# Kernel tuning notes

Hardware: AMD Instinct MI355X
Metric: run time of the kernel (lower is better)

## Reference

```python
import jax, jax.numpy as jnp
import numpy as np

B, C, N, DI, DC = 64, 32, 1152, 8, 16
ROUTINGS = 3


def squash(x, axis=-1):
    sq = jnp.sum(x * x, axis=axis, keepdims=True)
    scale = sq / (1.0 + sq) / jnp.sqrt(sq + 1e-07)
    return scale * x


def setup_inputs() -> dict:
    key = jax.random.key(0)
    k1, k2 = jax.random.split(key)
    inputs = jax.random.normal(k1, (B, N, DI), dtype=jnp.float32)
    # Xavier-uniform init for W[n_caps, n_in, d_cap, d_in]; fan computed over last two dims
    limit = float(np.sqrt(6.0 / (DC + DI)))
    W = jax.random.uniform(k2, (C, N, DC, DI), dtype=jnp.float32, minval=-limit, maxval=limit)
    return {"inputs": inputs, "W": W}


def reference(inputs, W):
    # inputs_hat[b,c,n,i] = sum_j W[c,n,i,j] * inputs[b,n,j]
    inputs_hat = jnp.einsum('cnij,bnj->bcni', W, inputs)  # [B,C,N,DC]
    b = jnp.zeros((B, C, N), dtype=inputs_hat.dtype)
    outputs = None
    for i in range(ROUTINGS):
        c = jax.nn.softmax(b, axis=1)                      # over output capsules
        s = jnp.einsum('bcn,bcni->bci', c, inputs_hat)     # weighted sum over input caps
        outputs = squash(s)                                # [B,C,DC]
        if i < ROUTINGS - 1:
            agreement = jnp.einsum('bci,bcni->bcn', outputs, inputs_hat)
            b = b + agreement
    return outputs
```

## Files before the change

kernel.cpp:

```cpp
#include <hip/hip_runtime.h>
#include <hip/hip_bf16.h>

#define B_  64
#define C_  32
#define N_  1152
#define DI_ 8
#define DC_ 16
#define NCH 3
#define NSLOT 128
#define STH 512

static __device__ __forceinline__ unsigned pkbf(float a, float b) {
    __hip_bfloat162 t = __float22bfloat162_rn(make_float2(a, b));
    return *reinterpret_cast<unsigned*>(&t);
}
static __device__ __forceinline__ float ubf_lo(unsigned u) {
    union { unsigned u; float f; } x; x.u = u << 16; return x.f;
}
static __device__ __forceinline__ float ubf_hi(unsigned u) {
    union { unsigned u; float f; } x; x.u = u & 0xffff0000u; return x.f;
}

__global__ __launch_bounds__(STH, 2) void caps_hat(
    const float* __restrict__ X, const float* __restrict__ W,
    uint4* __restrict__ hatg, float* __restrict__ partials)
{
    __shared__ float wlds[NCH * 64 * 64];
    __shared__ float xlds[NCH * 16 * 8];

    const int bg   = blockIdx.x & 3;
    const int slot = blockIdx.x >> 2;
    const int tid  = threadIdx.x;
    const int w    = tid >> 6;
    const int lane = tid & 63;
    const int c    = lane & 31;
    const int h    = lane >> 5;
    const int bl0  = w * 2;
    const int le   = 2 * c + h;
    const int sw   = c & 7;

    float acc[2][8];
#pragma unroll
    for (int bq = 0; bq < 2; bq++)
#pragma unroll
        for (int r = 0; r < 8; r++) acc[bq][r] = 0.f;

    for (int cc = 0; cc < 3; cc++) {
        if (cc) __syncthreads();
        const int n0 = (slot + cc * NSLOT) * NCH;

        for (int G = tid; G < NCH * 1024; G += STH) {
            const int nl = G >> 10, f = (G >> 4) & 63, q = G & 15;
            const int wc = f >> 1, wh = f & 1;
            const float4 v = *(const float4*)(W + (size_t)(wc * N_ + n0 + nl) * 128 + wh * 64 + q * 4);
            *(float4*)(wlds + (nl * 64 + f) * 64 + (q ^ (wc & 7)) * 4) = v;
        }
        if (tid < NCH * 32) {
            const int nl = tid >> 5, bl = (tid >> 1) & 15, qx = tid & 1;
            const float4 v = *(const float4*)(X + (size_t)((bg * 16 + bl) * N_ + n0 + nl) * DI_ + qx * 4);
            *(float4*)(xlds + (nl * 16 + bl) * 8 + qx * 4) = v;
        }
        __syncthreads();

#pragma unroll
        for (int nl = 0; nl < NCH; nl++) {
            float4 xa[2], xb[2];
#pragma unroll
            for (int bq = 0; bq < 2; bq++) {
                const float* xp = xlds + (nl * 16 + bl0 + bq) * 8;
                xa[bq] = *(const float4*)xp;
                xb[bq] = *(const float4*)(xp + 4);
            }
            float hv[2][8];
            const float* frag = wlds + (nl * 64 + le) * 64;
#pragma unroll
            for (int r = 0; r < 8; r++) {
                const int pa = ((2 * r) ^ sw) * 4;
                const int pb = pa ^ 4;
                const float4 wa = *(const float4*)(frag + pa);
                const float4 wb = *(const float4*)(frag + pb);
#pragma unroll
                for (int bq = 0; bq < 2; bq++) {
                    hv[bq][r] = wa.x * xa[bq].x + wa.y * xa[bq].y + wa.z * xa[bq].z + wa.w * xa[bq].w
                              + wb.x * xb[bq].x + wb.y * xb[bq].y + wb.z * xb[bq].z + wb.w * xb[bq].w;
                }
            }
#pragma unroll
            for (int bq = 0; bq < 2; bq++) {
                uint4 hq;
                hq.x = pkbf(hv[bq][0], hv[bq][1]);
                hq.y = pkbf(hv[bq][2], hv[bq][3]);
                hq.z = pkbf(hv[bq][4], hv[bq][5]);
                hq.w = pkbf(hv[bq][6], hv[bq][7]);
                const int b = bg * 16 + bl0 + bq;
                hatg[(size_t)(b * N_ + n0 + nl) * 64 + le] = hq;
#pragma unroll
                for (int r = 0; r < 8; r++) acc[bq][r] += hv[bq][r];
            }
        }
    }

    float* pout = partials + (size_t)(bg * NSLOT + slot) * (16 * 512);
#pragma unroll
    for (int bq = 0; bq < 2; bq++) {
        float* pb = pout + (bl0 + bq) * 512 + le * 8;
        *(float4*)pb       = make_float4(acc[bq][0]*0.03125f, acc[bq][1]*0.03125f,
                                         acc[bq][2]*0.03125f, acc[bq][3]*0.03125f);
        *(float4*)(pb + 4) = make_float4(acc[bq][4]*0.03125f, acc[bq][5]*0.03125f,
                                         acc[bq][6]*0.03125f, acc[bq][7]*0.03125f);
    }
}

__global__ __launch_bounds__(STH, 2) void caps_route(
    const uint4* __restrict__ hatg, const float* __restrict__ accb,
    float* __restrict__ p2)
{
    const int b    = blockIdx.x >> 3;
    const int oct  = blockIdx.x & 7;
    const int tid  = threadIdx.x;
    const int w    = tid >> 6;
    const int lane = tid & 63;
    const int c    = lane & 31;
    const int h    = lane >> 5;
    const int le   = 2 * c + h;

    const float* ap = accb + (size_t)b * 512 + le * 8;
    const float4 a0 = *(const float4*)ap;
    const float4 a1 = *(const float4*)(ap + 4);

    float acc[8] = {0.f,0.f,0.f,0.f,0.f,0.f,0.f,0.f};
    const uint4* hb = hatg + (size_t)(b * N_ + oct * 144) * 64 + le;

    for (int k = 0; k < 6; k++) {
        uint4 v[3];
#pragma unroll
        for (int u = 0; u < 3; u++)
            v[u] = hb[(size_t)(w + 8 * (3 * k + u)) * 64];
#pragma unroll
        for (int u = 0; u < 3; u++) {
            float hv[8];
            hv[0] = ubf_lo(v[u].x); hv[1] = ubf_hi(v[u].x);
            hv[2] = ubf_lo(v[u].y); hv[3] = ubf_hi(v[u].y);
            hv[4] = ubf_lo(v[u].z); hv[5] = ubf_hi(v[u].z);
            hv[6] = ubf_lo(v[u].w); hv[7] = ubf_hi(v[u].w);
            float lg = hv[0]*a0.x + hv[1]*a0.y + hv[2]*a0.z + hv[3]*a0.w
                     + hv[4]*a1.x + hv[5]*a1.y + hv[6]*a1.z + hv[7]*a1.w;
            lg += __shfl_xor(lg, 32, 64);
            const float e = __expf(lg);
            float s = e;
#pragma unroll
            for (int m = 16; m >= 1; m >>= 1) s += __shfl_xor(s, m, 64);
            const float sc = e * __builtin_amdgcn_rcpf(s);
#pragma unroll
            for (int r = 0; r < 8; r++) acc[r] += sc * hv[r];
        }
    }
    float* pb = p2 + ((size_t)(b * 8 + oct) * 8 + w) * 512 + le * 8;
    *(float4*)pb       = make_float4(acc[0], acc[1], acc[2], acc[3]);
    *(float4*)(pb + 4) = make_float4(acc[4], acc[5], acc[6], acc[7]);
}

__global__ __launch_bounds__(256) void caps_r1(
    const float* __restrict__ partials, float* __restrict__ accb,
    float* __restrict__ out, int t)
{
    const int b   = blockIdx.x >> 2;
    const int q   = blockIdx.x & 3;
    const int tid = threadIdx.x;
    const int e   = q * 128 + (tid >> 1);
    const int p   = tid & 1;
    const int bg  = b >> 4, bl = b & 15;
    const float* base = partials + (size_t)bg * NSLOT * 8192 + (size_t)bl * 512 + e;
    float v = 0.f;
#pragma unroll 8
    for (int ch = p; ch < NSLOT; ch += 2)
        v += base[(size_t)ch * 8192];
    v += __shfl_xor(v, 1, 64);
    float sq = v * v;
#pragma unroll
    for (int m = 2; m <= 16; m <<= 1) sq += __shfl_xor(sq, m, 64);
    const float scale = sq / (1.f + sq) * rsqrtf(sq + 1e-7f);
    const float ov = v * scale;
    if (p == 0) {
        const int oidx = b * 512 + e;
        if (t == 2) out[oidx] = ov;
        else        accb[oidx] = (t == 0) ? ov : (accb[oidx] + ov);
    }
}

__global__ __launch_bounds__(512) void caps_r2(
    const float* __restrict__ p2, float* __restrict__ accb,
    float* __restrict__ out, int t)
{
    const int b = blockIdx.x;
    const int e = threadIdx.x;
    const float* base = p2 + (size_t)b * 32768 + e;
    float v = 0.f;
#pragma unroll 16
    for (int s = 0; s < 64; s++) v += base[s * 512];
    float sq = v * v;
#pragma unroll
    for (int m = 1; m <= 8; m <<= 1) sq += __shfl_xor(sq, m, 64);
    const float scale = sq / (1.f + sq) * rsqrtf(sq + 1e-7f);
    const float ov = v * scale;
    const int oidx = b * 512 + e;
    if (t == 2) out[oidx] = ov;
    else        accb[oidx] += ov;
}

__global__ __launch_bounds__(STH, 2) void caps_s_fb(
    const float* __restrict__ X, const float* __restrict__ W,
    const float* __restrict__ aout, float* __restrict__ partials, int t)
{
    __shared__ float wlds[NCH * 64 * 64];
    __shared__ float xlds[NCH * 16 * 8];
    const int bg = blockIdx.x & 3, slot = blockIdx.x >> 2;
    const int tid = threadIdx.x, w = tid >> 6, lane = tid & 63;
    const int c = lane & 31, h = lane >> 5, bl0 = w * 2, sw = c & 7;
    float areg[2][8] = {};
    if (t > 0) {
#pragma unroll
        for (int bq = 0; bq < 2; bq++) {
            const float* ap = aout + (size_t)(bg * 16 + bl0 + bq) * 512 + c * 16 + h * 8;
            const float4 a0 = *(const float4*)ap; const float4 a1 = *(const float4*)(ap + 4);
            areg[bq][0]=a0.x; areg[bq][1]=a0.y; areg[bq][2]=a0.z; areg[bq][3]=a0.w;
            areg[bq][4]=a1.x; areg[bq][5]=a1.y; areg[bq][6]=a1.z; areg[bq][7]=a1.w;
        }
    }
    float acc[2][8];
#pragma unroll
    for (int bq = 0; bq < 2; bq++)
#pragma unroll
        for (int r = 0; r < 8; r++) acc[bq][r] = 0.f;
    for (int cc = 0; cc < 3; cc++) {
        if (cc) __syncthreads();
        const int n0 = (slot + cc * NSLOT) * NCH;
        for (int G = tid; G < NCH * 1024; G += STH) {
            const int nl = G >> 10, f = (G >> 4) & 63, q = G & 15;
            const int wc = f >> 1, wh = f & 1;
            const float4 v = *(const float4*)(W + (size_t)(wc * N_ + n0 + nl) * 128 + wh * 64 + q * 4);
            *(float4*)(wlds + (nl * 64 + f) * 64 + (q ^ (wc & 7)) * 4) = v;
        }
        if (tid < NCH * 32) {
            const int nl = tid >> 5, bl = (tid >> 1) & 15, qx = tid & 1;
            const float4 v = *(const float4*)(X + (size_t)((bg * 16 + bl) * N_ + n0 + nl) * DI_ + qx * 4);
            *(float4*)(xlds + (nl * 16 + bl) * 8 + qx * 4) = v;
        }
        __syncthreads();
#pragma unroll
        for (int nl = 0; nl < NCH; nl++) {
            float4 xa[2], xb[2];
#pragma unroll
            for (int bq = 0; bq < 2; bq++) {
                const float* xp = xlds + (nl * 16 + bl0 + bq) * 8;
                xa[bq] = *(const float4*)xp; xb[bq] = *(const float4*)(xp + 4);
            }
            float hat[2][8];
            const float* frag = wlds + (nl * 64 + 2 * c + h) * 64;
#pragma unroll
            for (int r = 0; r < 8; r++) {
                const int pa = ((2 * r) ^ sw) * 4; const int pb = pa ^ 4;
                const float4 wa = *(const float4*)(frag + pa);
                const float4 wb = *(const float4*)(frag + pb);
#pragma unroll
                for (int bq = 0; bq < 2; bq++)
                    hat[bq][r] = wa.x*xa[bq].x + wa.y*xa[bq].y + wa.z*xa[bq].z + wa.w*xa[bq].w
                               + wb.x*xb[bq].x + wb.y*xb[bq].y + wb.z*xb[bq].z + wb.w*xb[bq].w;
            }
#pragma unroll
            for (int bq = 0; bq < 2; bq++) {
                float softc;
                if (t > 0) {
                    float lg = hat[bq][0]*areg[bq][0] + hat[bq][1]*areg[bq][1]
                             + hat[bq][2]*areg[bq][2] + hat[bq][3]*areg[bq][3]
                             + hat[bq][4]*areg[bq][4] + hat[bq][5]*areg[bq][5]
                             + hat[bq][6]*areg[bq][6] + hat[bq][7]*areg[bq][7];
                    lg += __shfl_xor(lg, 32, 64);
                    const float e = __expf(lg);
                    float s = e;
#pragma unroll
                    for (int m = 16; m >= 1; m >>= 1) s += __shfl_xor(s, m, 64);
                    softc = e / s;
                } else softc = 1.0f / 32.0f;
#pragma unroll
                for (int r = 0; r < 8; r++) acc[bq][r] += softc * hat[bq][r];
            }
        }
    }
    float* pout = partials + (size_t)(bg * NSLOT + slot) * (16 * 512);
#pragma unroll
    for (int bq = 0; bq < 2; bq++) {
        float* pb = pout + (bl0 + bq) * 512 + c * 16 + h * 8;
        *(float4*)pb       = make_float4(acc[bq][0], acc[bq][1], acc[bq][2], acc[bq][3]);
        *(float4*)(pb + 4) = make_float4(acc[bq][4], acc[bq][5], acc[bq][6], acc[bq][7]);
    }
}

extern "C" void kernel_launch(void* const* d_in, const int* in_sizes, int n_in,
                              void* d_out, int out_size, void* d_ws, size_t ws_size,
                              hipStream_t stream) {
    const float* X = (const float*)d_in[0];
    const float* W = (const float*)d_in[1];
    float* out = (float*)d_out;

    const size_t hat_b = (size_t)B_ * N_ * 512 * 2;
    const size_t p1_b  = (size_t)512 * 8192 * 4;
    const size_t p2_b  = (size_t)B_ * 64 * 512 * 4;
    const size_t acc_b = (size_t)B_ * 512 * 4;

    if (ws_size >= hat_b + p1_b + p2_b + acc_b) {
        char* ws = (char*)d_ws;
        uint4* hatg = (uint4*)ws;
        float* p1   = (float*)(ws + hat_b);
        float* p2   = (float*)(ws + hat_b + p1_b);
        float* accb = (float*)(ws + hat_b + p1_b + p2_b);
        caps_hat  <<<512, STH, 0, stream>>>(X, W, hatg, p1);
        caps_r1   <<<256, 256, 0, stream>>>(p1, accb, out, 0);
        caps_route<<<512, STH, 0, stream>>>(hatg, accb, p2);
        caps_r2   <<<64, 512, 0, stream>>>(p2, accb, out, 1);
        caps_route<<<512, STH, 0, stream>>>(hatg, accb, p2);
        caps_r2   <<<64, 512, 0, stream>>>(p2, accb, out, 2);
    } else {
        float* partials = (float*)d_ws;
        float* accb = partials + (size_t)512 * 8192;
        for (int t = 0; t < 3; t++) {
            caps_s_fb<<<512, STH, 0, stream>>>(X, W, accb, partials, t);
            caps_r1  <<<256, 256, 0, stream>>>(partials, accb, out, t);
        }
    }
}
```

Baseline: 153.4 us.

## Store hat in fp16, double batch per block, reduce route partials in LDS

The cached inputs_hat is now stored as fp16 instead of bf16, and caps_hat processes 32 batches per block (4 per wave) over half as many blocks. This halves the W tile loads from global memory and raises per-load reuse. caps_route reduces its 8 wave partials in shared memory before writing, and its occupancy hint rises to 6. That shrinks p2 writes and the r2 reduction eightfold. The costs are more registers in caps_hat, fewer blocks to fill the GPU, and fp16 range and precision limits on hat values.

```diff
diff --git a/kernel.cpp b/kernel.cpp
--- a/kernel.cpp
+++ b/kernel.cpp
@@ -1,5 +1,6 @@
 #include <hip/hip_runtime.h>
 #include <hip/hip_bf16.h>
+#include <hip/hip_fp16.h>
 
 #define B_  64
 #define C_  32
@@ -10,38 +11,36 @@
 #define NSLOT 128
 #define STH 512
 
-static __device__ __forceinline__ unsigned pkbf(float a, float b) {
-    __hip_bfloat162 t = __float22bfloat162_rn(make_float2(a, b));
+static __device__ __forceinline__ unsigned pkh(float a, float b) {
+    __half2 t = __float22half2_rn(make_float2(a, b));
     return *reinterpret_cast<unsigned*>(&t);
 }
-static __device__ __forceinline__ float ubf_lo(unsigned u) {
-    union { unsigned u; float f; } x; x.u = u << 16; return x.f;
-}
-static __device__ __forceinline__ float ubf_hi(unsigned u) {
-    union { unsigned u; float f; } x; x.u = u & 0xffff0000u; return x.f;
+static __device__ __forceinline__ float2 uph(unsigned u) {
+    __half2 h; *reinterpret_cast<unsigned*>(&h) = u;
+    return __half22float2(h);
 }
 
 __global__ __launch_bounds__(STH, 2) void caps_hat(
     const float* __restrict__ X, const float* __restrict__ W,
-    uint4* __restrict__ hatg, float* __restrict__ partials)
+    uint4* __restrict__ hatg, float* __restrict__ p1)
 {
     __shared__ float wlds[NCH * 64 * 64];
-    __shared__ float xlds[NCH * 16 * 8];
-
-    const int bg   = blockIdx.x & 3;
-    const int slot = blockIdx.x >> 2;
+    __shared__ float xlds[NCH * 32 * 8];
+
+    const int bg   = blockIdx.x & 1;
+    const int slot = blockIdx.x >> 1;
     const int tid  = threadIdx.x;
     const int w    = tid >> 6;
     const int lane = tid & 63;
     const int c    = lane & 31;
     const int h    = lane >> 5;
-    const int bl0  = w * 2;
+    const int bl0  = w * 4;
     const int le   = 2 * c + h;
     const int sw   = c & 7;
 
-    float acc[2][8];
-#pragma unroll
-    for (int bq = 0; bq < 2; bq++)
+    float acc[4][8];
+#pragma unroll
+    for (int bq = 0; bq < 4; bq++)
 #pragma unroll
         for (int r = 0; r < 8; r++) acc[bq][r] = 0.f;
 
@@ -55,54 +54,57 @@
             const float4 v = *(const float4*)(W + (size_t)(wc * N_ + n0 + nl) * 128 + wh * 64 + q * 4);
             *(float4*)(wlds + (nl * 64 + f) * 64 + (q ^ (wc & 7)) * 4) = v;
         }
-        if (tid < NCH * 32) {
-            const int nl = tid >> 5, bl = (tid >> 1) & 15, qx = tid & 1;
-            const float4 v = *(const float4*)(X + (size_t)((bg * 16 + bl) * N_ + n0 + nl) * DI_ + qx * 4);
-            *(float4*)(xlds + (nl * 16 + bl) * 8 + qx * 4) = v;
+        if (tid < NCH * 64) {
+            const int nl = tid >> 6, bl = (tid >> 1) & 31, qx = tid & 1;
+            const float4 v = *(const float4*)(X + (size_t)((bg * 32 + bl) * N_ + n0 + nl) * DI_ + qx * 4);
+            *(float4*)(xlds + (nl * 32 + bl) * 8 + qx * 4) = v;
         }
         __syncthreads();
 
 #pragma unroll
         for (int nl = 0; nl < NCH; nl++) {
-            float4 xa[2], xb[2];
-#pragma unroll
-            for (int bq = 0; bq < 2; bq++) {
-                const float* xp = xlds + (nl * 16 + bl0 + bq) * 8;
+            float4 xa[4], xb[4];
+#pragma unroll
+            for (int bq = 0; bq < 4; bq++) {
+                const float* xp = xlds + (nl * 32 + bl0 + bq) * 8;
                 xa[bq] = *(const float4*)xp;
                 xb[bq] = *(const float4*)(xp + 4);
             }
-            float hv[2][8];
+            uint4 hq[4];
             const float* frag = wlds + (nl * 64 + le) * 64;
 #pragma unroll
-            for (int r = 0; r < 8; r++) {
-                const int pa = ((2 * r) ^ sw) * 4;
-                const int pb = pa ^ 4;
-                const float4 wa = *(const float4*)(frag + pa);
-                const float4 wb = *(const float4*)(frag + pb);
-#pragma unroll
-                for (int bq = 0; bq < 2; bq++) {
-                    hv[bq][r] = wa.x * xa[bq].x + wa.y * xa[bq].y + wa.z * xa[bq].z + wa.w * xa[bq].w
-                              + wb.x * xb[bq].x + wb.y * xb[bq].y + wb.z * xb[bq].z + wb.w * xb[bq].w;
+            for (int rp = 0; rp < 4; rp++) {
+                const int r0 = 2 * rp, r1 = r0 + 1;
+                const int pa0 = ((2 * r0) ^ sw) * 4;
+                const int pb0 = pa0 ^ 4;
+                const int pa1 = ((2 * r1) ^ sw) * 4;
+                const int pb1 = pa1 ^ 4;
+                const float4 wa0 = *(const float4*)(frag + pa0);
+                const float4 wb0 = *(const float4*)(frag + pb0);
+                const float4 wa1 = *(const float4*)(frag + pa1);
+                const float4 wb1 = *(const float4*)(frag + pb1);
+#pragma unroll
+                for (int bq = 0; bq < 4; bq++) {
+                    const float hv0 = wa0.x*xa[bq].x + wa0.y*xa[bq].y + wa0.z*xa[bq].z + wa0.w*xa[bq].w
+                                    + wb0.x*xb[bq].x + wb0.y*xb[bq].y + wb0.z*xb[bq].z + wb0.w*xb[bq].w;
+                    const float hv1 = wa1.x*xa[bq].x + wa1.y*xa[bq].y + wa1.z*xa[bq].z + wa1.w*xa[bq].w
+                                    + wb1.x*xb[bq].x + wb1.y*xb[bq].y + wb1.z*xb[bq].z + wb1.w*xb[bq].w;
+                    acc[bq][r0] += hv0;
+                    acc[bq][r1] += hv1;
+                    (&hq[bq].x)[rp] = pkh(hv0, hv1);
                 }
             }
 #pragma unroll
-            for (int bq = 0; bq < 2; bq++) {
-                uint4 hq;
-                hq.x = pkbf(hv[bq][0], hv[bq][1]);
-                hq.y = pkbf(hv[bq][2], hv[bq][3]);
-                hq.z = pkbf(hv[bq][4], hv[bq][5]);
-                hq.w = pkbf(hv[bq][6], hv[bq][7]);
-                const int b = bg * 16 + bl0 + bq;
-                hatg[(size_t)(b * N_ + n0 + nl) * 64 + le] = hq;
-#pragma unroll
-                for (int r = 0; r < 8; r++) acc[bq][r] += hv[bq][r];
-            }
-        }
-    }
-
-    float* pout = partials + (size_t)(bg * NSLOT + slot) * (16 * 512);
-#pragma unroll
-    for (int bq = 0; bq < 2; bq++) {
+            for (int bq = 0; bq < 4; bq++) {
+                const int b = bg * 32 + bl0 + bq;
+                hatg[(size_t)(b * N_ + n0 + nl) * 64 + le] = hq[bq];
+            }
+        }
+    }
+
+    float* pout = p1 + (size_t)(bg * NSLOT + slot) * (32 * 512);
+#pragma unroll
+    for (int bq = 0; bq < 4; bq++) {
         float* pb = pout + (bl0 + bq) * 512 + le * 8;
         *(float4*)pb       = make_float4(acc[bq][0]*0.03125f, acc[bq][1]*0.03125f,
                                          acc[bq][2]*0.03125f, acc[bq][3]*0.03125f);
@@ -111,10 +113,11 @@
     }
 }
 
-__global__ __launch_bounds__(STH, 2) void caps_route(
+__global__ __launch_bounds__(STH, 6) void caps_route(
     const uint4* __restrict__ hatg, const float* __restrict__ accb,
     float* __restrict__ p2)
 {
+    __shared__ float red[8 * 512];
     const int b    = blockIdx.x >> 3;
     const int oct  = blockIdx.x & 7;
     const int tid  = threadIdx.x;
@@ -138,29 +141,170 @@
             v[u] = hb[(size_t)(w + 8 * (3 * k + u)) * 64];
 #pragma unroll
         for (int u = 0; u < 3; u++) {
-            float hv[8];
-            hv[0] = ubf_lo(v[u].x); hv[1] = ubf_hi(v[u].x);
-            hv[2] = ubf_lo(v[u].y); hv[3] = ubf_hi(v[u].y);
-            hv[4] = ubf_lo(v[u].z); hv[5] = ubf_hi(v[u].z);
-            hv[6] = ubf_lo(v[u].w); hv[7] = ubf_hi(v[u].w);
-            float lg = hv[0]*a0.x + hv[1]*a0.y + hv[2]*a0.z + hv[3]*a0.w
-                     + hv[4]*a1.x + hv[5]*a1.y + hv[6]*a1.z + hv[7]*a1.w;
+            const float2 f0 = uph(v[u].x);
+            const float2 f1 = uph(v[u].y);
+            const float2 f2 = uph(v[u].z);
+            const float2 f3 = uph(v[u].w);
+            float lg = f0.x*a0.x + f0.y*a0.y + f1.x*a0.z + f1.y*a0.w
+                     + f2.x*a1.x + f2.y*a1.y + f3.x*a1.z + f3.y*a1.w;
             lg += __shfl_xor(lg, 32, 64);
             const float e = __expf(lg);
             float s = e;
 #pragma unroll
             for (int m = 16; m >= 1; m >>= 1) s += __shfl_xor(s, m, 64);
             const float sc = e * __builtin_amdgcn_rcpf(s);
-#pragma unroll
-            for (int r = 0; r < 8; r++) acc[r] += sc * hv[r];
-        }
-    }
-    float* pb = p2 + ((size_t)(b * 8 + oct) * 8 + w) * 512 + le * 8;
-    *(float4*)pb       = make_float4(acc[0], acc[1], acc[2], acc[3]);
-    *(float4*)(pb + 4) = make_float4(acc[4], acc[5], acc[6], acc[7]);
+            acc[0] += sc * f0.x; acc[1] += sc * f0.y;
+            acc[2] += sc * f1.x; acc[3] += sc * f1.y;
+            acc[4] += sc * f2.x; acc[5] += sc * f2.y;
+            acc[6] += sc * f3.x; acc[7] += sc * f3.y;
+        }
+    }
+    *(float4*)(red + w * 512 + le * 8)     = make_float4(acc[0], acc[1], acc[2], acc[3]);
+    *(float4*)(red + w * 512 + le * 8 + 4) = make_float4(acc[4], acc[5], acc[6], acc[7]);
+    __syncthreads();
+    float vs = 0.f;
+#pragma unroll
+    for (int s = 0; s < 8; s++) vs += red[s * 512 + tid];
+    p2[(size_t)(b * 8 + oct) * 512 + tid] = vs;
 }
 
 __global__ __launch_bounds__(256) void caps_r1(
+    const float* __restrict__ p1, float* __restrict__ accb,
+    float* __restrict__ out, int t)
+{
+    const int b   = blockIdx.x >> 2;
+    const int q   = blockIdx.x & 3;
+    const int tid = threadIdx.x;
+    const int e   = q * 128 + (tid >> 1);
+    const int p   = tid & 1;
+    const int bg  = b >> 5, bl = b & 31;
+    const float* base = p1 + (size_t)bg * NSLOT * 16384 + (size_t)bl * 512 + e;
+    float v = 0.f;
+#pragma unroll 8
+    for (int ch = p; ch < NSLOT; ch += 2)
+        v += base[(size_t)ch * 16384];
+    v += __shfl_xor(v, 1, 64);
+    float sq = v * v;
+#pragma unroll
+    for (int m = 2; m <= 16; m <<= 1) sq += __shfl_xor(sq, m, 64);
+    const float scale = sq / (1.f + sq) * rsqrtf(sq + 1e-7f);
+    const float ov = v * scale;
+    if (p == 0) {
+        const int oidx = b * 512 + e;
+        if (t == 2) out[oidx] = ov;
+        else        accb[oidx] = (t == 0) ? ov : (accb[oidx] + ov);
+    }
+}
+
+__global__ __launch_bounds__(512) void caps_r2(
+    const float* __restrict__ p2, float* __restrict__ accb,
+    float* __restrict__ out, int t)
+{
+    const int b = blockIdx.x;
+    const int e = threadIdx.x;
+    const float* base = p2 + (size_t)b * 4096 + e;
+    float v = 0.f;
+#pragma unroll
+    for (int s = 0; s < 8; s++) v += base[s * 512];
+    float sq = v * v;
+#pragma unroll
+    for (int m = 1; m <= 8; m <<= 1) sq += __shfl_xor(sq, m, 64);
+    const float scale = sq / (1.f + sq) * rsqrtf(sq + 1e-7f);
+    const float ov = v * scale;
+    const int oidx = b * 512 + e;
+    if (t == 2) out[oidx] = ov;
+    else        accb[oidx] += ov;
+}
+
+__global__ __launch_bounds__(STH, 2) void caps_s_fb(
+    const float* __restrict__ X, const float* __restrict__ W,
+    const float* __restrict__ aout, float* __restrict__ partials, int t)
+{
+    __shared__ float wlds[NCH * 64 * 64];
+    __shared__ float xlds[NCH * 16 * 8];
+    const int bg = blockIdx.x & 3, slot = blockIdx.x >> 2;
+    const int tid = threadIdx.x, w = tid >> 6, lane = tid & 63;
+    const int c = lane & 31, h = lane >> 5, bl0 = w * 2, sw = c & 7;
+    float areg[2][8] = {};
+    if (t > 0) {
+#pragma unroll
+        for (int bq = 0; bq < 2; bq++) {
+            const float* ap = aout + (size_t)(bg * 16 + bl0 + bq) * 512 + c * 16 + h * 8;
+            const float4 a0 = *(const float4*)ap; const float4 a1 = *(const float4*)(ap + 4);
+            areg[bq][0]=a0.x; areg[bq][1]=a0.y; areg[bq][2]=a0.z; areg[bq][3]=a0.w;
+            areg[bq][4]=a1.x; areg[bq][5]=a1.y; areg[bq][6]=a1.z; areg[bq][7]=a1.w;
+        }
+    }
+    float acc[2][8];
+#pragma unroll
+    for (int bq = 0; bq < 2; bq++)
+#pragma unroll
+        for (int r = 0; r < 8; r++) acc[bq][r] = 0.f;
+    for (int cc = 0; cc < 3; cc++) {
+        if (cc) __syncthreads();
+        const int n0 = (slot + cc * NSLOT) * NCH;
+        for (int G = tid; G < NCH * 1024; G += STH) {
+            const int nl = G >> 10, f = (G >> 4) & 63, q = G & 15;
+            const int wc = f >> 1, wh = f & 1;
+            const float4 v = *(const float4*)(W + (size_t)(wc * N_ + n0 + nl) * 128 + wh * 64 + q * 4);
+            *(float4*)(wlds + (nl * 64 + f) * 64 + (q ^ (wc & 7)) * 4) = v;
+        }
+        if (tid < NCH * 32) {
+            const int nl = tid >> 5, bl = (tid >> 1) & 15, qx = tid & 1;
+            const float4 v = *(const float4*)(X + (size_t)((bg * 16 + bl) * N_ + n0 + nl) * DI_ + qx * 4);
+            *(float4*)(xlds + (nl * 16 + bl) * 8 + qx * 4) = v;
+        }
+        __syncthreads();
+#pragma unroll
+        for (int nl = 0; nl < NCH; nl++) {
+            float4 xa[2], xb[2];
+#pragma unroll
+            for (int bq = 0; bq < 2; bq++) {
+                const float* xp = xlds + (nl * 16 + bl0 + bq) * 8;
+                xa[bq] = *(const float4*)xp; xb[bq] = *(const float4*)(xp + 4);
+            }
+            float hat[2][8];
+            const float* frag = wlds + (nl * 64 + 2 * c + h) * 64;
+#pragma unroll
+            for (int r = 0; r < 8; r++) {
+                const int pa = ((2 * r) ^ sw) * 4; const int pb = pa ^ 4;
+                const float4 wa = *(const float4*)(frag + pa);
+                const float4 wb = *(const float4*)(frag + pb);
+#pragma unroll
+                for (int bq = 0; bq < 2; bq++)
+                    hat[bq][r] = wa.x*xa[bq].x + wa.y*xa[bq].y + wa.z*xa[bq].z + wa.w*xa[bq].w
+                               + wb.x*xb[bq].x + wb.y*xb[bq].y + wb.z*xb[bq].z + wb.w*xb[bq].w;
+            }
+#pragma unroll
+            for (int bq = 0; bq < 2; bq++) {
+                float softc;
+                if (t > 0) {
+                    float lg = hat[bq][0]*areg[bq][0] + hat[bq][1]*areg[bq][1]
+                             + hat[bq][2]*areg[bq][2] + hat[bq][3]*areg[bq][3]
+                             + hat[bq][4]*areg[bq][4] + hat[bq][5]*areg[bq][5]
+                             + hat[bq][6]*areg[bq][6] + hat[bq][7]*areg[bq][7];
+                    lg += __shfl_xor(lg, 32, 64);
+                    const float e = __expf(lg);
+                    float s = e;
+#pragma unroll
+                    for (int m = 16; m >= 1; m >>= 1) s += __shfl_xor(s, m, 64);
+                    softc = e / s;
+                } else softc = 1.0f / 32.0f;
+#pragma unroll
+                for (int r = 0; r < 8; r++) acc[bq][r] += softc * hat[bq][r];
+            }
+        }
+    }
+    float* pout = partials + (size_t)(bg * NSLOT + slot) * (16 * 512);
+#pragma unroll
+    for (int bq = 0; bq < 2; bq++) {
+        float* pb = pout + (bl0 + bq) * 512 + c * 16 + h * 8;
+        *(float4*)pb       = make_float4(acc[bq][0], acc[bq][1], acc[bq][2], acc[bq][3]);
+        *(float4*)(pb + 4) = make_float4(acc[bq][4], acc[bq][5], acc[bq][6], acc[bq][7]);
+    }
+}
+
+__global__ __launch_bounds__(256) void caps_r1_fb(
     const float* __restrict__ partials, float* __restrict__ accb,
     float* __restrict__ out, int t)
 {
@@ -188,114 +332,6 @@
     }
 }
 
-__global__ __launch_bounds__(512) void caps_r2(
-    const float* __restrict__ p2, float* __restrict__ accb,
-    float* __restrict__ out, int t)
-{
-    const int b = blockIdx.x;
-    const int e = threadIdx.x;
-    const float* base = p2 + (size_t)b * 32768 + e;
-    float v = 0.f;
-#pragma unroll 16
-    for (int s = 0; s < 64; s++) v += base[s * 512];
-    float sq = v * v;
-#pragma unroll
-    for (int m = 1; m <= 8; m <<= 1) sq += __shfl_xor(sq, m, 64);
-    const float scale = sq / (1.f + sq) * rsqrtf(sq + 1e-7f);
-    const float ov = v * scale;
-    const int oidx = b * 512 + e;
-    if (t == 2) out[oidx] = ov;
-    else        accb[oidx] += ov;
-}
-
-__global__ __launch_bounds__(STH, 2) void caps_s_fb(
-    const float* __restrict__ X, const float* __restrict__ W,
-    const float* __restrict__ aout, float* __restrict__ partials, int t)
-{
-    __shared__ float wlds[NCH * 64 * 64];
-    __shared__ float xlds[NCH * 16 * 8];
-    const int bg = blockIdx.x & 3, slot = blockIdx.x >> 2;
-    const int tid = threadIdx.x, w = tid >> 6, lane = tid & 63;
-    const int c = lane & 31, h = lane >> 5, bl0 = w * 2, sw = c & 7;
-    float areg[2][8] = {};
-    if (t > 0) {
-#pragma unroll
-        for (int bq = 0; bq < 2; bq++) {
-            const float* ap = aout + (size_t)(bg * 16 + bl0 + bq) * 512 + c * 16 + h * 8;
-            const float4 a0 = *(const float4*)ap; const float4 a1 = *(const float4*)(ap + 4);
-            areg[bq][0]=a0.x; areg[bq][1]=a0.y; areg[bq][2]=a0.z; areg[bq][3]=a0.w;
-            areg[bq][4]=a1.x; areg[bq][5]=a1.y; areg[bq][6]=a1.z; areg[bq][7]=a1.w;
-        }
-    }
-    float acc[2][8];
-#pragma unroll
-    for (int bq = 0; bq < 2; bq++)
-#pragma unroll
-        for (int r = 0; r < 8; r++) acc[bq][r] = 0.f;
-    for (int cc = 0; cc < 3; cc++) {
-        if (cc) __syncthreads();
-        const int n0 = (slot + cc * NSLOT) * NCH;
-        for (int G = tid; G < NCH * 1024; G += STH) {
-            const int nl = G >> 10, f = (G >> 4) & 63, q = G & 15;
-            const int wc = f >> 1, wh = f & 1;
-            const float4 v = *(const float4*)(W + (size_t)(wc * N_ + n0 + nl) * 128 + wh * 64 + q * 4);
-            *(float4*)(wlds + (nl * 64 + f) * 64 + (q ^ (wc & 7)) * 4) = v;
-        }
-        if (tid < NCH * 32) {
-            const int nl = tid >> 5, bl = (tid >> 1) & 15, qx = tid & 1;
-            const float4 v = *(const float4*)(X + (size_t)((bg * 16 + bl) * N_ + n0 + nl) * DI_ + qx * 4);
-            *(float4*)(xlds + (nl * 16 + bl) * 8 + qx * 4) = v;
-        }
-        __syncthreads();
-#pragma unroll
-        for (int nl = 0; nl < NCH; nl++) {
-            float4 xa[2], xb[2];
-#pragma unroll
-            for (int bq = 0; bq < 2; bq++) {
-                const float* xp = xlds + (nl * 16 + bl0 + bq) * 8;
-                xa[bq] = *(const float4*)xp; xb[bq] = *(const float4*)(xp + 4);
-            }
-            float hat[2][8];
-            const float* frag = wlds + (nl * 64 + 2 * c + h) * 64;
-#pragma unroll
-            for (int r = 0; r < 8; r++) {
-                const int pa = ((2 * r) ^ sw) * 4; const int pb = pa ^ 4;
-                const float4 wa = *(const float4*)(frag + pa);
-                const float4 wb = *(const float4*)(frag + pb);
-#pragma unroll
-                for (int bq = 0; bq < 2; bq++)
-                    hat[bq][r] = wa.x*xa[bq].x + wa.y*xa[bq].y + wa.z*xa[bq].z + wa.w*xa[bq].w
-                               + wb.x*xb[bq].x + wb.y*xb[bq].y + wb.z*xb[bq].z + wb.w*xb[bq].w;
-            }
-#pragma unroll
-            for (int bq = 0; bq < 2; bq++) {
-                float softc;
-                if (t > 0) {
-                    float lg = hat[bq][0]*areg[bq][0] + hat[bq][1]*areg[bq][1]
-                             + hat[bq][2]*areg[bq][2] + hat[bq][3]*areg[bq][3]
-                             + hat[bq][4]*areg[bq][4] + hat[bq][5]*areg[bq][5]
-                             + hat[bq][6]*areg[bq][6] + hat[bq][7]*areg[bq][7];
-                    lg += __shfl_xor(lg, 32, 64);
-                    const float e = __expf(lg);
-                    float s = e;
-#pragma unroll
-                    for (int m = 16; m >= 1; m >>= 1) s += __shfl_xor(s, m, 64);
-                    softc = e / s;
-                } else softc = 1.0f / 32.0f;
-#pragma unroll
-                for (int r = 0; r < 8; r++) acc[bq][r] += softc * hat[bq][r];
-            }
-        }
-    }
-    float* pout = partials + (size_t)(bg * NSLOT + slot) * (16 * 512);
-#pragma unroll
-    for (int bq = 0; bq < 2; bq++) {
-        float* pb = pout + (bl0 + bq) * 512 + c * 16 + h * 8;
-        *(float4*)pb       = make_float4(acc[bq][0], acc[bq][1], acc[bq][2], acc[bq][3]);
-        *(float4*)(pb + 4) = make_float4(acc[bq][4], acc[bq][5], acc[bq][6], acc[bq][7]);
-    }
-}
-
 extern "C" void kernel_launch(void* const* d_in, const int* in_sizes, int n_in,
                               void* d_out, int out_size, void* d_ws, size_t ws_size,
                               hipStream_t stream) {
@@ -304,8 +340,8 @@
     float* out = (float*)d_out;
 
     const size_t hat_b = (size_t)B_ * N_ * 512 * 2;
-    const size_t p1_b  = (size_t)512 * 8192 * 4;
-    const size_t p2_b  = (size_t)B_ * 64 * 512 * 4;
+    const size_t p1_b  = (size_t)256 * 16384 * 4;
+    const size_t p2_b  = (size_t)B_ * 8 * 512 * 4;
     const size_t acc_b = (size_t)B_ * 512 * 4;
 
     if (ws_size >= hat_b + p1_b + p2_b + acc_b) {
@@ -314,7 +350,7 @@
         float* p1   = (float*)(ws + hat_b);
         float* p2   = (float*)(ws + hat_b + p1_b);
         float* accb = (float*)(ws + hat_b + p1_b + p2_b);
-        caps_hat  <<<512, STH, 0, stream>>>(X, W, hatg, p1);
+        caps_hat  <<<256, STH, 0, stream>>>(X, W, hatg, p1);
         caps_r1   <<<256, 256, 0, stream>>>(p1, accb, out, 0);
         caps_route<<<512, STH, 0, stream>>>(hatg, accb, p2);
         caps_r2   <<<64, 512, 0, stream>>>(p2, accb, out, 1);
@@ -325,7 +361,7 @@
         float* accb = partials + (size_t)512 * 8192;
         for (int t = 0; t < 3; t++) {
             caps_s_fb<<<512, STH, 0, stream>>>(X, W, accb, partials, t);
-            caps_r1  <<<256, 256, 0, stream>>>(partials, accb, out, t);
-        }
-    }
-}
+            caps_r1_fb<<<256, 256, 0, stream>>>(partials, accb, out, t);
+        }
+    }
+}
```

Result: slower. 190.9 us (+24.4%).
